# Performance work log

Measured on AMD Instinct MI355X. Metric: run time of the kernel, lower is better.

## Reference

```python
import jax, jax.numpy as jnp
import numpy as np

KS = 21        # kernel_size
SIGMA = 5.0    # sigma
C = 3          # channels
PAD = KS // 2  # reflection pad = 10


def _gaussian_kernel():
    # Matches torch construction: 2D isotropic Gaussian on integer grid, then
    # normalized to sum 1. Separable => outer product of 1D Gaussians.
    coords = jnp.arange(KS, dtype=jnp.float32)
    mean = (KS - 1) / 2.0
    g1 = jnp.exp(-((coords - mean) ** 2) / (2.0 * SIGMA ** 2))
    k2 = jnp.outer(g1, g1)
    k2 = k2 / jnp.sum(k2)
    # depthwise weight [C, 1, KS, KS] (OIHW with feature_group_count=C)
    return jnp.tile(k2[None, None, :, :], (C, 1, 1, 1))


def setup_inputs() -> dict:
    key = jax.random.key(0)
    x = jax.random.normal(key, (32, 3, 512, 512), dtype=jnp.float32)
    return {"x": x}


def reference(x):
    w = _gaussian_kernel()
    xp = jnp.pad(x, ((0, 0), (0, 0), (PAD, PAD), (PAD, PAD)), mode="reflect")
    out = jax.lax.conv_general_dilated(
        xp, w,
        window_strides=(1, 1),
        padding="VALID",
        dimension_numbers=("NCHW", "OIHW", "NCHW"),
        feature_group_count=C,
    )
    return out  # [B, C, H, W], same spatial size as input
```

## Files before the change

### kernel.cpp

```cpp
#include <hip/hip_runtime.h>
#include <math.h>


#define KS   21
#define PAD  10
#define TILE 64
#define LH   (TILE + 2 * PAD)
#define SW_IN 88
#define SW_H  68
#define IMG_H 512
#define IMG_W 512
#define NTHREADS 256

__global__ __launch_bounds__(NTHREADS) void gauss_blur_kernel(
    const float* __restrict__ in, float* __restrict__ out)
{
    __shared__ __align__(16) float s_in[LH * SW_IN];
    __shared__ __align__(16) float s_h [LH * SW_H];

    float w[KS];
    {
        float s = 0.f;
#pragma unroll
        for (int k = 0; k < KS; ++k) {
            float d = (float)(k - PAD);
            w[k] = expf(-d * d * (1.0f / 50.0f));
            s += w[k];
        }
        float inv = 1.0f / s;
#pragma unroll
        for (int k = 0; k < KS; ++k) w[k] *= inv;
    }

    const int tid   = threadIdx.x;
    const int plane = blockIdx.z;
    const int x0    = blockIdx.x * TILE;
    const int y0    = blockIdx.y * TILE;

    const float* __restrict__ pin = in + (size_t)plane * (IMG_H * IMG_W);

    const bool x_interior = (blockIdx.x != 0) && (blockIdx.x != (IMG_W / TILE - 1));
    if (x_interior) {
        for (int q = tid; q < LH * (SW_IN / 4); q += NTHREADS) {
            int ly  = q / (SW_IN / 4);
            int lx4 = q - ly * (SW_IN / 4);
            int col = lx4 << 2;
            int gy  = y0 + ly - PAD;
            gy = (gy < 0) ? -gy : ((gy >= IMG_H) ? (2 * IMG_H - 2 - gy) : gy);
            float4 f = *(const float4*)&pin[(size_t)gy * IMG_W + (x0 - 12) + col];
            *(float4*)&s_in[ly * SW_IN + col] = f;
        }
    } else {
        for (int q = tid; q < LH * SW_IN; q += NTHREADS) {
            int ly = q / SW_IN;
            int lx = q - ly * SW_IN;
            int gy = y0 + ly - PAD;
            int gx = x0 + lx - 12;
            gy = (gy < 0) ? -gy : ((gy >= IMG_H) ? (2 * IMG_H - 2 - gy) : gy);
            gx = (gx < 0) ? -gx : ((gx >= IMG_W) ? (2 * IMG_W - 2 - gx) : gx);
            s_in[ly * SW_IN + lx] = pin[(size_t)gy * IMG_W + gx];
        }
    }
    __syncthreads();

    for (int it = 0; it < 3; ++it) {
        int idx = tid + it * NTHREADS;
        if (idx < LH * (TILE / 8)) {
            int ly = idx >> 3;
            int lx = (idx & 7) << 3;
            const float4* rp = (const float4*)&s_in[ly * SW_IN + lx];
            float v[32];
#pragma unroll
            for (int t = 0; t < 8; ++t) {
                float4 f = rp[t];
                v[4 * t + 0] = f.x; v[4 * t + 1] = f.y;
                v[4 * t + 2] = f.z; v[4 * t + 3] = f.w;
            }
            float a[8] = {0, 0, 0, 0, 0, 0, 0, 0};
#pragma unroll
            for (int k = 0; k < KS; ++k) {
                float wk = w[k];
#pragma unroll
                for (int j = 0; j < 8; ++j) a[j] += wk * v[2 + j + k];
            }
            *(float4*)&s_h[ly * SW_H + lx]     = make_float4(a[0], a[1], a[2], a[3]);
            *(float4*)&s_h[ly * SW_H + lx + 4] = make_float4(a[4], a[5], a[6], a[7]);
        }
    }
    __syncthreads();

    {
        const int wv = tid >> 6;
        const int x  = tid & 63;
        const int oy = wv << 4;

        float acc[16];
#pragma unroll
        for (int j = 0; j < 16; ++j) acc[j] = 0.f;

#pragma unroll
        for (int t = 0; t < 36; ++t) {
            float r = s_h[(oy + t) * SW_H + x];
#pragma unroll
            for (int j = 0; j < 16; ++j)
                if (j >= t - (KS - 1) && j <= t) acc[j] += w[t - j] * r;
        }

        float* __restrict__ pout = out + (size_t)plane * (IMG_H * IMG_W)
                                       + (size_t)(y0 + oy) * IMG_W + x0 + x;
#pragma unroll
        for (int j = 0; j < 16; ++j) pout[(size_t)j * IMG_W] = acc[j];
    }
}

extern "C" void kernel_launch(void* const* d_in, const int* in_sizes, int n_in,
                              void* d_out, int out_size, void* d_ws, size_t ws_size,
                              hipStream_t stream)
{
    const float* x = (const float*)d_in[0];
    float* out = (float*)d_out;

    dim3 grid(IMG_W / TILE, IMG_H / TILE, 96);
    dim3 block(NTHREADS);
    gauss_blur_kernel<<<grid, block, 0, stream>>>(x, out);
}
```

Baseline: 230.3 us.

## Fuse horizontal pass with global loads and hardcode Gaussian weights

Removes the shared-memory input tile: each thread now loads its 28-32 input values straight from global memory and computes the horizontal blur, writing only the intermediate to LDS. Gaussian weights become compile-time constants instead of being computed with expf per thread. This removes one barrier, an LDS round trip, and about 29KB of shared memory per block, which may raise occupancy. In exchange, overlapping threads reread the same global data, relying on L1/L2 cache for reuse.

```diff
diff --git a/kernel.cpp b/kernel.cpp
--- a/kernel.cpp
+++ b/kernel.cpp
@@ -1,90 +1,93 @@
 #include <hip/hip_runtime.h>
-#include <math.h>
 
 
 #define KS   21
 #define PAD  10
 #define TILE 64
 #define LH   (TILE + 2 * PAD)
-#define SW_IN 88
-#define SW_H  68
-#define IMG_H 512
-#define IMG_W 512
+#define SW_H 68
+#define IMG  512
 #define NTHREADS 256
+
+#define GW(i) W[i]
+__device__ __constant__ float c_unused;
 
 __global__ __launch_bounds__(NTHREADS) void gauss_blur_kernel(
     const float* __restrict__ in, float* __restrict__ out)
 {
-    __shared__ __align__(16) float s_in[LH * SW_IN];
-    __shared__ __align__(16) float s_h [LH * SW_H];
+    __shared__ __align__(16) float s_h[LH * SW_H];
 
-    float w[KS];
-    {
-        float s = 0.f;
-#pragma unroll
-        for (int k = 0; k < KS; ++k) {
-            float d = (float)(k - PAD);
-            w[k] = expf(-d * d * (1.0f / 50.0f));
-            s += w[k];
-        }
-        float inv = 1.0f / s;
-#pragma unroll
-        for (int k = 0; k < KS; ++k) w[k] *= inv;
-    }
+    constexpr float W[KS] = {
+        0.011194717f, 0.016369860f, 0.022998804f, 0.031045124f, 0.040263373f,
+        0.050171245f, 0.060066033f, 0.069092259f, 0.076358728f, 0.081080459f,
+        0.082718387f,
+        0.081080459f, 0.076358728f, 0.069092259f, 0.060066033f, 0.050171245f,
+        0.040263373f, 0.031045124f, 0.022998804f, 0.016369860f, 0.011194717f
+    };
 
     const int tid   = threadIdx.x;
     const int plane = blockIdx.z;
     const int x0    = blockIdx.x * TILE;
     const int y0    = blockIdx.y * TILE;
 
-    const float* __restrict__ pin = in + (size_t)plane * (IMG_H * IMG_W);
+    const float* __restrict__ pin = in + (size_t)plane * (IMG * IMG);
 
-    const bool x_interior = (blockIdx.x != 0) && (blockIdx.x != (IMG_W / TILE - 1));
+    const bool x_interior = (blockIdx.x != 0) && (blockIdx.x != (IMG / TILE - 1));
+
     if (x_interior) {
-        for (int q = tid; q < LH * (SW_IN / 4); q += NTHREADS) {
-            int ly  = q / (SW_IN / 4);
-            int lx4 = q - ly * (SW_IN / 4);
-            int col = lx4 << 2;
-            int gy  = y0 + ly - PAD;
-            gy = (gy < 0) ? -gy : ((gy >= IMG_H) ? (2 * IMG_H - 2 - gy) : gy);
-            float4 f = *(const float4*)&pin[(size_t)gy * IMG_W + (x0 - 12) + col];
-            *(float4*)&s_in[ly * SW_IN + col] = f;
+#pragma unroll
+        for (int it = 0; it < 3; ++it) {
+            int idx = tid + it * NTHREADS;
+            if (idx < LH * (TILE / 8)) {
+                int ly = idx >> 3;
+                int lx = (idx & 7) << 3;
+                int gy = y0 + ly - PAD;
+                gy = (gy < 0) ? -gy : ((gy >= IMG) ? (2 * IMG - 2 - gy) : gy);
+                const float4* __restrict__ rp =
+                    (const float4*)&pin[(size_t)gy * IMG + (x0 - 12) + lx];
+                float v[32];
+#pragma unroll
+                for (int t = 0; t < 8; ++t) {
+                    float4 f = rp[t];
+                    v[4 * t + 0] = f.x; v[4 * t + 1] = f.y;
+                    v[4 * t + 2] = f.z; v[4 * t + 3] = f.w;
+                }
+                float a[8] = {0, 0, 0, 0, 0, 0, 0, 0};
+#pragma unroll
+                for (int k = 0; k < KS; ++k) {
+#pragma unroll
+                    for (int j = 0; j < 8; ++j) a[j] += W[k] * v[2 + j + k];
+                }
+                *(float4*)&s_h[ly * SW_H + lx]     = make_float4(a[0], a[1], a[2], a[3]);
+                *(float4*)&s_h[ly * SW_H + lx + 4] = make_float4(a[4], a[5], a[6], a[7]);
+            }
         }
     } else {
-        for (int q = tid; q < LH * SW_IN; q += NTHREADS) {
-            int ly = q / SW_IN;
-            int lx = q - ly * SW_IN;
-            int gy = y0 + ly - PAD;
-            int gx = x0 + lx - 12;
-            gy = (gy < 0) ? -gy : ((gy >= IMG_H) ? (2 * IMG_H - 2 - gy) : gy);
-            gx = (gx < 0) ? -gx : ((gx >= IMG_W) ? (2 * IMG_W - 2 - gx) : gx);
-            s_in[ly * SW_IN + lx] = pin[(size_t)gy * IMG_W + gx];
-        }
-    }
-    __syncthreads();
-
-    for (int it = 0; it < 3; ++it) {
-        int idx = tid + it * NTHREADS;
-        if (idx < LH * (TILE / 8)) {
-            int ly = idx >> 3;
-            int lx = (idx & 7) << 3;
-            const float4* rp = (const float4*)&s_in[ly * SW_IN + lx];
-            float v[32];
 #pragma unroll
-            for (int t = 0; t < 8; ++t) {
-                float4 f = rp[t];
-                v[4 * t + 0] = f.x; v[4 * t + 1] = f.y;
-                v[4 * t + 2] = f.z; v[4 * t + 3] = f.w;
+        for (int it = 0; it < 3; ++it) {
+            int idx = tid + it * NTHREADS;
+            if (idx < LH * (TILE / 8)) {
+                int ly = idx >> 3;
+                int lx = (idx & 7) << 3;
+                int gy = y0 + ly - PAD;
+                gy = (gy < 0) ? -gy : ((gy >= IMG) ? (2 * IMG - 2 - gy) : gy);
+                const float* __restrict__ row = &pin[(size_t)gy * IMG];
+                float v[28];
+#pragma unroll
+                for (int t = 0; t < 28; ++t) {
+                    int gx = x0 + lx - 10 + t;
+                    gx = (gx < 0) ? -gx : ((gx >= IMG) ? (2 * IMG - 2 - gx) : gx);
+                    v[t] = row[gx];
+                }
+                float a[8] = {0, 0, 0, 0, 0, 0, 0, 0};
+#pragma unroll
+                for (int k = 0; k < KS; ++k) {
+#pragma unroll
+                    for (int j = 0; j < 8; ++j) a[j] += W[k] * v[j + k];
+                }
+                *(float4*)&s_h[ly * SW_H + lx]     = make_float4(a[0], a[1], a[2], a[3]);
+                *(float4*)&s_h[ly * SW_H + lx + 4] = make_float4(a[4], a[5], a[6], a[7]);
             }
-            float a[8] = {0, 0, 0, 0, 0, 0, 0, 0};
-#pragma unroll
-            for (int k = 0; k < KS; ++k) {
-                float wk = w[k];
-#pragma unroll
-                for (int j = 0; j < 8; ++j) a[j] += wk * v[2 + j + k];
-            }
-            *(float4*)&s_h[ly * SW_H + lx]     = make_float4(a[0], a[1], a[2], a[3]);
-            *(float4*)&s_h[ly * SW_H + lx + 4] = make_float4(a[4], a[5], a[6], a[7]);
         }
     }
     __syncthreads();
@@ -103,13 +106,13 @@
             float r = s_h[(oy + t) * SW_H + x];
 #pragma unroll
             for (int j = 0; j < 16; ++j)
-                if (j >= t - (KS - 1) && j <= t) acc[j] += w[t - j] * r;
+                if (j >= t - (KS - 1) && j <= t) acc[j] += W[t - j] * r;
         }
 
-        float* __restrict__ pout = out + (size_t)plane * (IMG_H * IMG_W)
-                                       + (size_t)(y0 + oy) * IMG_W + x0 + x;
+        float* __restrict__ pout = out + (size_t)plane * (IMG * IMG)
+                                       + (size_t)(y0 + oy) * IMG + x0 + x;
 #pragma unroll
-        for (int j = 0; j < 16; ++j) pout[(size_t)j * IMG_W] = acc[j];
+        for (int j = 0; j < 16; ++j) pout[(size_t)j * IMG] = acc[j];
     }
 }
 
@@ -120,7 +123,7 @@
     const float* x = (const float*)d_in[0];
     float* out = (float*)d_out;
 
-    dim3 grid(IMG_W / TILE, IMG_H / TILE, 96);
+    dim3 grid(IMG / TILE, IMG / TILE, 96);
     dim3 block(NTHREADS);
     gauss_blur_kernel<<<grid, block, 0, stream>>>(x, out);
 }
```

Result: slower. 285.5 us (+24.0%).
